# Kernel tuning notes

Measured on AMD Instinct MI355X. Metric: run time of the kernel, lower is better.

## Reference

```python
import jax, jax.numpy as jnp
import numpy as np

# ---- Config constants (from DGM Config) ----
DIM = 20        # number of assets; inputs have DIM+1 cols (last is time)
DELTA = 0.01    # finite-difference step / covariance scale
RHO = 0.5       # asset correlation
MC = 32         # Config.mc_num
N = 2048        # interior points (inputs holds 2*N rows)
UNITS = 128     # Config.unit_num
LAYERS = 3      # Config.layer_num
SIG = 0.2       # Config._sig
MU = 0.05       # Config._mu
R = 0.05        # Config._r

_cov = DELTA * (np.full((DIM, DIM), RHO, dtype=np.float64) + (1.0 - RHO) * np.eye(DIM))
L_TRIL = jnp.asarray(np.linalg.cholesky(_cov).astype(np.float32))  # (DIM, DIM) lower-tri


def setup_inputs() -> dict:
    key = jax.random.key(0)
    ks = jax.random.split(key, 20)
    d = DIM + 1
    u = lambda k, shp: jax.random.uniform(k, shp, jnp.float32, -0.05, 0.05)
    inp = {
        # strictly positive inputs so boundary prod**(1/DIM) is well-defined
        "inputs": jax.random.uniform(ks[0], (2 * N, d), jnp.float32, 0.1, 1.0),
        "eps": jax.random.normal(ks[1], (MC, N, DIM), jnp.float32),
        "w1": u(ks[2], (d, UNITS)), "b1": u(ks[3], (UNITS,)),
        "uzl": u(ks[4], (d, UNITS)), "wzl": u(ks[5], (UNITS, UNITS)), "bzl": u(ks[6], (UNITS,)),
        "ugl": u(ks[7], (d, UNITS)), "wgl": u(ks[8], (UNITS, UNITS)), "bgl": u(ks[9], (UNITS,)),
        "url": u(ks[10], (d, UNITS)), "wrl": u(ks[11], (UNITS, UNITS)), "brl": u(ks[12], (UNITS,)),
        "uhl": u(ks[13], (d, UNITS)), "whl": u(ks[14], (UNITS, UNITS)), "bhl": u(ks[15], (UNITS,)),
        "w": u(ks[16], (UNITS, 1)), "b": u(ks[17], (1,)),
    }
    return inp


def _value(x, w1, b1, uzl, wzl, bzl, ugl, wgl, bgl, url, wrl, brl, uhl, whl, bhl, w, b):
    # DGM gated residual network; x: (..., DIM+1) -> (..., 1)
    act = jnp.tanh
    s = act(x @ w1 + b1)
    for _ in range(LAYERS):
        z = act(x @ uzl + s @ wzl + bzl)
        g = act(x @ ugl + s @ wgl + bgl)
        r = act(x @ url + s @ wrl + brl)
        h = act(x @ uhl + (s * r) @ whl + bhl)
        s = (1.0 - g) * h + z * s
    return s @ w + b


def reference(inputs, eps, w1, b1, uzl, wzl, bzl, ugl, wgl, bgl, url, wrl, brl,
              uhl, whl, bhl, w, b):
    params = (w1, b1, uzl, wzl, bzl, ugl, wgl, bgl, url, wrl, brl, uhl, whl, bhl, w, b)
    val = lambda x: _value(x, *params)
    x1, x2 = jnp.split(inputs, 2, axis=0)          # interior / boundary points

    # first-order grad of value w.r.t. interior inputs
    fprime = jax.grad(lambda x: val(x).sum())(x1)  # (N, DIM+1)
    drift = jnp.concatenate([MU * x1[:, :-1], jnp.ones((x1.shape[0], 1), x1.dtype)], axis=1)
    term1_1 = jnp.sum(drift * fprime, axis=1)      # (N,)

    # correlated MVN perturbations (reparameterized): loc + eps @ L^T
    loc = x1[:, :-1]                               # (N, DIM)
    sample = loc[None, :, :] + jnp.einsum('mnd,kd->mnk', eps, L_TRIL)  # (MC, N, DIM)
    xdiff = sample * (SIG * loc)[None, :, :]
    violation = jnp.concatenate([xdiff, jnp.zeros((MC, x1.shape[0], 1), x1.dtype)], axis=2)
    xplus = x1[None, :, :] + violation             # (MC, N, DIM+1)

    fprime_plus = jax.grad(lambda x: val(x).sum())(xplus)  # (MC, N, DIM+1)
    term1_2 = jnp.sum(
        jnp.mean((fprime_plus - fprime[None, :, :]) / DELTA * violation, axis=0), axis=1)

    # boundary residual: value - payoff (geometric-mean call payoff)
    payoff = jax.nn.relu(jnp.power(jnp.prod(x2[:, :-1], axis=1), 1.0 / DIM))
    term2 = jnp.squeeze(val(x2), -1) - payoff

    interior = term1_1 + 0.5 * term1_2 - R * jnp.squeeze(val(x1), -1)
    return jnp.concatenate([interior, term2], axis=0)  # (2N,)
```

## Files before the change

### kernel.cpp

```cpp
#include <hip/hip_runtime.h>
#include <math.h>

#define DIMN 20
#define DD 21
#define NN 2048
#define MCN 32
#define UNITS 128
#define SIGC 0.2f
#define MUC 0.05f
#define RC 0.05f
#define DELTAC 0.01f

#define TM 32
#define KCH 16
#define KC3 8
#define PTOT (NN + MCN*NN + NN)
#define NBLK (PTOT/TM)

#define OFF_L 0
#define OFF_WT 512
#define OFF_UZGR (OFF_WT + 4*16384)
#define OFF_WZGR (OFF_UZGR + 8192)
#define OFF_FP1  (OFF_WZGR + 49152)
#define OFF_VAL1 (OFF_FP1 + NN*DD)
#define OFF_VAL2 (OFF_VAL1 + NN)
#define OFF_T12  (OFF_VAL2 + NN)
#define OFF_GATES (OFF_T12 + NN)

#define ST_S1 0
#define ST_Z1 4096
#define ST_G1 8192
#define ST_R1 12288
#define ST_Z2 16384
#define ST_G2 20480
#define ST_R2 24576
#define GB_STRIDE 28672

#define L_TOT_SG 19776
#define L_TOT_RC 23872

#define ELT44(...) _Pragma("unroll") for (int p = 0; p < 4; p++){ _Pragma("unroll") for (int jj = 0; jj < 4; jj++){ __VA_ARGS__; } }

__device__ __forceinline__ int offq(int row, int p0){
    return row*32 + ((p0 + 4*(row&7)) & 31);
}
__device__ __forceinline__ int offs(int row, int p){
    return row*32 + (((p & 28) + 4*(row&7)) & 31) + (p & 3);
}

__device__ __forceinline__ void stageW(const float* __restrict__ g, float* wc, int units){
#if defined(__has_builtin) && __has_builtin(__builtin_amdgcn_global_load_lds)
    int lane = threadIdx.x & 63, wid = threadIdx.x >> 6;
    for (int base = wid*64; base < units; base += 256){
        int u = base + lane;
        if (u < units)
            __builtin_amdgcn_global_load_lds(
                (const __attribute__((address_space(1))) unsigned int*)(g) + (size_t)u*4,
                (__attribute__((address_space(3))) unsigned int*)(wc) + (size_t)base*4,
                16, 0, 0);
    }
#else
    int t = threadIdx.x;
    for (int u = t; u < units; u += 256){
        float4 v = *(const float4*)(g + u*4);
        *(float4*)(wc + u*4) = v;
    }
#endif
}

#define FMA16(acc, s4, w4) \
  acc[0][0]=fmaf(s4.x,w4.x,acc[0][0]); acc[0][1]=fmaf(s4.x,w4.y,acc[0][1]); \
  acc[0][2]=fmaf(s4.x,w4.z,acc[0][2]); acc[0][3]=fmaf(s4.x,w4.w,acc[0][3]); \
  acc[1][0]=fmaf(s4.y,w4.x,acc[1][0]); acc[1][1]=fmaf(s4.y,w4.y,acc[1][1]); \
  acc[1][2]=fmaf(s4.y,w4.z,acc[1][2]); acc[1][3]=fmaf(s4.y,w4.w,acc[1][3]); \
  acc[2][0]=fmaf(s4.z,w4.x,acc[2][0]); acc[2][1]=fmaf(s4.z,w4.y,acc[2][1]); \
  acc[2][2]=fmaf(s4.z,w4.z,acc[2][2]); acc[2][3]=fmaf(s4.z,w4.w,acc[2][3]); \
  acc[3][0]=fmaf(s4.w,w4.x,acc[3][0]); acc[3][1]=fmaf(s4.w,w4.y,acc[3][1]); \
  acc[3][2]=fmaf(s4.w,w4.z,acc[3][2]); acc[3][3]=fmaf(s4.w,w4.w,acc[3][3]);

__device__ __forceinline__ void mm_acc(const float* __restrict__ gW, int K,
    const float* __restrict__ vec, float acc[4][4], float* __restrict__ Wc,
    int jg, int p0)
{
    int nch = (K + KCH - 1) / KCH;
    {
        int r0 = (K < KCH) ? K : KCH;
        stageW(gW, Wc, r0*32);
    }
    for (int c = 0; c < nch; c++){
        __syncthreads();
        if (c + 1 < nch){
            int c0n = (c+1)*KCH;
            int rn = K - c0n; if (rn > KCH) rn = KCH;
            stageW(gW + c0n*UNITS, Wc + ((c+1)&1)*KCH*UNITS, rn*32);
        }
        int c0 = c*KCH;
        int rows = K - c0; if (rows > KCH) rows = KCH;
        const float* wb = Wc + (c&1)*KCH*UNITS;
        if (rows == KCH){
            #pragma unroll 4
            for (int kk = 0; kk < KCH; kk++){
                int k = c0 + kk;
                float4 w4 = *(const float4*)(wb + kk*UNITS + 4*jg);
                float4 s4 = *(const float4*)(vec + offq(k, p0));
                FMA16(acc, s4, w4)
            }
        } else {
            for (int kk = 0; kk < rows; kk++){
                int k = c0 + kk;
                float4 w4 = *(const float4*)(wb + kk*UNITS + 4*jg);
                float4 s4 = *(const float4*)(vec + offq(k, p0));
                FMA16(acc, s4, w4)
            }
        }
    }
    __syncthreads();
}

__device__ __forceinline__ void mm3_acc(const float* __restrict__ gW, int K,
    const float* __restrict__ vec, float az[4][4], float ag[4][4], float ar[4][4],
    float* __restrict__ Wc, int jg, int p0)
{
    int nch = (K + KC3 - 1) / KC3;
    {
        int r0 = (K < KC3) ? K : KC3;
        stageW(gW, Wc, r0*96);
    }
    for (int c = 0; c < nch; c++){
        __syncthreads();
        if (c + 1 < nch){
            int c0n = (c+1)*KC3;
            int rn = K - c0n; if (rn > KC3) rn = KC3;
            stageW(gW + c0n*384, Wc + ((c+1)&1)*(KC3*384), rn*96);
        }
        int c0 = c*KC3;
        int rows = K - c0; if (rows > KC3) rows = KC3;
        const float* wb = Wc + (c&1)*(KC3*384);
        if (rows == KC3){
            #pragma unroll 2
            for (int kk = 0; kk < KC3; kk++){
                int k = c0 + kk;
                const float* wrow = wb + kk*384 + 4*jg;
                float4 s4  = *(const float4*)(vec + offq(k, p0));
                float4 wz4 = *(const float4*)(wrow);
                float4 wg4 = *(const float4*)(wrow + 128);
                float4 wr4 = *(const float4*)(wrow + 256);
                FMA16(az, s4, wz4)
                FMA16(ag, s4, wg4)
                FMA16(ar, s4, wr4)
            }
        } else {
            for (int kk = 0; kk < rows; kk++){
                int k = c0 + kk;
                const float* wrow = wb + kk*384 + 4*jg;
                float4 s4  = *(const float4*)(vec + offq(k, p0));
                float4 wz4 = *(const float4*)(wrow);
                float4 wg4 = *(const float4*)(wrow + 128);
                float4 wr4 = *(const float4*)(wrow + 256);
                FMA16(az, s4, wz4)
                FMA16(ag, s4, wg4)
                FMA16(ar, s4, wr4)
            }
        }
    }
    __syncthreads();
}

__device__ __forceinline__ void write_own(float* buf, const float v[4][4], int j0, int p0){
    #pragma unroll
    for (int jj = 0; jj < 4; jj++){
        int j = j0 + jj;
        float4 q = make_float4(v[0][jj], v[1][jj], v[2][jj], v[3][jj]);
        *(float4*)(buf + offq(j, p0)) = q;
    }
}
__device__ __forceinline__ void read_own(const float* buf, float v[4][4], int j0, int p0){
    #pragma unroll
    for (int jj = 0; jj < 4; jj++){
        int j = j0 + jj;
        float4 q = *(const float4*)(buf + offq(j, p0));
        v[0][jj]=q.x; v[1][jj]=q.y; v[2][jj]=q.z; v[3][jj]=q.w;
    }
}
__device__ __forceinline__ void stash_w(float* buf, const float v[4][4], int t){
    #pragma unroll
    for (int jj = 0; jj < 4; jj++)
        *(float4*)(buf + (jj*256 + t)*4) = make_float4(v[0][jj], v[1][jj], v[2][jj], v[3][jj]);
}
__device__ __forceinline__ void stash_r(const float* buf, float v[4][4], int t){
    #pragma unroll
    for (int jj = 0; jj < 4; jj++){
        float4 q = *(const float4*)(buf + (jj*256 + t)*4);
        v[0][jj]=q.x; v[1][jj]=q.y; v[2][jj]=q.z; v[3][jj]=q.w;
    }
}

__device__ __forceinline__ void gate_f(const float* __restrict__ U, const float* __restrict__ W,
    const float* __restrict__ bias, const float* __restrict__ xT, const float* __restrict__ Sin,
    float* __restrict__ Wc, float out[4][4], int jg, int p0, int j0)
{
    float acc[4][4];
    float4 b = *(const float4*)(bias + j0);
    #pragma unroll
    for (int p = 0; p < 4; p++){ acc[p][0]=b.x; acc[p][1]=b.y; acc[p][2]=b.z; acc[p][3]=b.w; }
    mm_acc(U, DD, xT, acc, Wc, jg, p0);
    mm_acc(W, UNITS, Sin, acc, Wc, jg, p0);
    #pragma unroll
    for (int p = 0; p < 4; p++)
        #pragma unroll
        for (int jj = 0; jj < 4; jj++) out[p][jj] = tanhf(acc[p][jj]);
}

__device__ __forceinline__ void gate3_f(const float* __restrict__ Uzgr, const float* __restrict__ Wzgr,
    const float* __restrict__ bz, const float* __restrict__ bg, const float* __restrict__ br,
    const float* __restrict__ xT, const float* __restrict__ Sin,
    float* __restrict__ Wc, float zt[4][4], float gt[4][4], float rt[4][4],
    int jg, int p0, int j0)
{
    float4 b0 = *(const float4*)(bz + j0);
    float4 b1 = *(const float4*)(bg + j0);
    float4 b2 = *(const float4*)(br + j0);
    #pragma unroll
    for (int p = 0; p < 4; p++){
        zt[p][0]=b0.x; zt[p][1]=b0.y; zt[p][2]=b0.z; zt[p][3]=b0.w;
        gt[p][0]=b1.x; gt[p][1]=b1.y; gt[p][2]=b1.z; gt[p][3]=b1.w;
        rt[p][0]=b2.x; rt[p][1]=b2.y; rt[p][2]=b2.z; rt[p][3]=b2.w;
    }
    mm3_acc(Uzgr, DD, xT, zt, gt, rt, Wc, jg, p0);
    mm3_acc(Wzgr, UNITS, Sin, zt, gt, rt, Wc, jg, p0);
    ELT44(zt[p][jj]=tanhf(zt[p][jj]); gt[p][jj]=tanhf(gt[p][jj]); rt[p][jj]=tanhf(rt[p][jj]))
}

__global__ void chol_kernel(float* __restrict__ Lout)
{
    if (threadIdx.x == 0 && blockIdx.x == 0) {
        const double beta = 0.01 * 0.5;
        const double diag = 0.01;
        double c[DIMN], d[DIMN];
        double S = 0.0;
        for (int j = 0; j < DIMN; j++){
            double dj = sqrt(diag - S);
            double cj = (beta - S) / dj;
            d[j] = dj; c[j] = cj;
            S += cj*cj;
        }
        for (int i = 0; i < DIMN; i++)
            for (int j = 0; j < DIMN; j++)
                Lout[i*DIMN + j] = (j < i) ? (float)c[j] : (j == i) ? (float)d[i] : 0.0f;
    }
}

__global__ void transpose_k(const float* __restrict__ wz, const float* __restrict__ wg,
                            const float* __restrict__ wr, const float* __restrict__ wh,
                            float* __restrict__ WT)
{
    int idx = blockIdx.x*256 + threadIdx.x;
    int q = idx >> 14, r2 = idx & 16383, k = r2 >> 7, j = r2 & 127;
    const float* src = (q==0)? wz : (q==1)? wg : (q==2)? wr : wh;
    WT[(q<<14) + j*UNITS + k] = src[k*UNITS + j];
}

__global__ void pack_zgr(const float* __restrict__ uz, const float* __restrict__ ug,
                         const float* __restrict__ ur,
                         const float* __restrict__ wz, const float* __restrict__ wg,
                         const float* __restrict__ wr,
                         float* __restrict__ Uzgr, float* __restrict__ Wzgr)
{
    int idx = blockIdx.x*256 + threadIdx.x;
    if (idx < 128*384){
        int k = idx/384, c = idx - k*384, g = c >> 7, j = c & 127;
        const float* s = (g==0)? wz : (g==1)? wg : wr;
        Wzgr[idx] = s[k*UNITS + j];
        return;
    }
    int i2 = idx - 128*384;
    if (i2 < 21*384){
        int k = i2/384, c = i2 - k*384, g = c >> 7, j = c & 127;
        const float* s = (g==0)? uz : (g==1)? ug : ur;
        Uzgr[i2] = s[k*UNITS + j];
    }
}

#define DGM_PARAMS \
    const float* __restrict__ inputs, const float* __restrict__ eps, \
    const float* __restrict__ w1, const float* __restrict__ b1, \
    const float* __restrict__ uz, const float* __restrict__ bz, \
    const float* __restrict__ ug, const float* __restrict__ bg, \
    const float* __restrict__ ur, const float* __restrict__ br, \
    const float* __restrict__ uh, const float* __restrict__ wh, const float* __restrict__ bh, \
    const float* __restrict__ wv, const float* __restrict__ bv, \
    const float* __restrict__ Lm, const float* __restrict__ WT, \
    const float* __restrict__ Uzgr, const float* __restrict__ Wzgr, \
    float* __restrict__ gws, \
    float* __restrict__ fp1, float* __restrict__ val1, float* __restrict__ val2, \
    float* __restrict__ t12acc

#define DGM_ARGS inputs, eps, w1, b1, uz, bz, ug, bg, ur, br, uh, wh, bh, wv, bv, \
    Lm, WT, Uzgr, Wzgr, gws, fp1, val1, val2, t12acc

template<int SG>
__device__ __forceinline__ void dgm_body(float* lds, DGM_PARAMS)
{
    float* S0 = lds;
    float* S1 = SG ? lds : lds + 4096;
    float* S2 = lds + (SG ? 4096 : 8192);
    float* Db = lds + (SG ? 8192 : 12288);
    float* Wc = lds + (SG ? 12288 : 16384);
    float* xT = lds + (SG ? 18432 : 22528);
    float* Vb = lds + (SG ? 19104 : 23200);

    const int t  = threadIdx.x;
    const int jg = t & 31;
    const int pg = t >> 5;
    const int p0 = pg * 4;
    const int j0 = jg * 4;
    const int P0 = blockIdx.x * TM;
    const int type = (P0 < NN) ? 0 : (P0 < NN + MCN*NN) ? 1 : 2;
    int base_n = 0, mrow = 0;
    if (type == 1){ int q = P0 - NN; mrow = q >> 11; base_n = q & (NN-1); }

    float* gb = gws + (size_t)blockIdx.x * GB_STRIDE;

    {
        int p = t & 31, kq = t >> 5;
        for (int ki = 0; ki < 3; ki++){
            int k = kq + 8*ki;
            if (k > DIMN) break;
            float xv;
            if (type == 0){
                xv = inputs[(P0 + p)*DD + k];
            } else if (type == 2){
                xv = inputs[(NN + (P0 - NN - MCN*NN) + p)*DD + k];
            } else {
                int n = base_n + p;
                float x1v = inputs[n*DD + k];
                if (k == DIMN) xv = x1v;
                else {
                    const float* ep = eps + (size_t)(mrow*NN + n)*DIMN;
                    float a = x1v;
                    for (int d = 0; d < DIMN; d++) a = fmaf(ep[d], Lm[k*DIMN + d], a);
                    float viol = a * (SIGC * x1v);
                    Vb[offs(k, p)] = viol;
                    xv = x1v + viol;
                }
            }
            xT[offs(k, p)] = xv;
        }
    }
    __syncthreads();

    float s_own[4][4];
    {
        float acc[4][4];
        float4 b = *(const float4*)(b1 + j0);
        #pragma unroll
        for (int p = 0; p < 4; p++){ acc[p][0]=b.x; acc[p][1]=b.y; acc[p][2]=b.z; acc[p][3]=b.w; }
        mm_acc(w1, DD, xT, acc, Wc, jg, p0);
        ELT44(s_own[p][jj] = tanhf(acc[p][jj]))
        write_own(S0, s_own, j0, p0);
        __syncthreads();
    }

    float zt[4][4], gt[4][4], rt[4][4], ht[4][4];

#define GATES(SIN, SMUL) \
    gate3_f(Uzgr, Wzgr, bz, bg, br, xT, SIN, Wc, zt, gt, rt, jg, p0, j0); \
    { float tt[4][4]; ELT44(tt[p][jj] = SMUL[p][jj]*rt[p][jj]) write_own(Db, tt, j0, p0); } \
    gate_f(uh, wh, bh, xT, Db, Wc, ht, jg, p0, j0);

#define FWD_LAYER(SIN) \
    GATES(SIN, s_own) \
    ELT44(s_own[p][jj] = (1.f - gt[p][jj])*ht[p][jj] + zt[p][jj]*s_own[p][jj])

    FWD_LAYER(S0)
    if (SG){ if (type != 2){
        stash_w(gb + ST_S1, s_own, t);
        stash_w(gb + ST_Z1, zt, t); stash_w(gb + ST_G1, gt, t); stash_w(gb + ST_R1, rt, t);
    } }
    else   { write_own(S1, s_own, j0, p0); }
    write_own(Db, s_own, j0, p0);

    FWD_LAYER(Db)
    if (SG && type != 2){
        stash_w(gb + ST_Z2, zt, t); stash_w(gb + ST_G2, gt, t); stash_w(gb + ST_R2, rt, t);
    }
    write_own(S2, s_own, j0, p0);

    FWD_LAYER(S2)

    {
        float4 wv4 = *(const float4*)(wv + j0);
        float vs[4];
        #pragma unroll
        for (int p = 0; p < 4; p++)
            vs[p] = s_own[p][0]*wv4.x + s_own[p][1]*wv4.y + s_own[p][2]*wv4.z + s_own[p][3]*wv4.w;
        __syncthreads();
        *(float4*)(Db + jg*32 + p0) = make_float4(vs[0], vs[1], vs[2], vs[3]);
        __syncthreads();
        if (t < TM){
            float v = bv[0];
            for (int j2 = 0; j2 < 32; j2++) v += Db[j2*32 + t];
            if (type == 0) val1[P0 + t] = v;
            else if (type == 2) val2[P0 + t - NN - MCN*NN] = v;
        }
        __syncthreads();
    }
    if (type == 2) return;

    float ds[4][4];
    {
        float4 wv4 = *(const float4*)(wv + j0);
        #pragma unroll
        for (int p = 0; p < 4; p++){ ds[p][0]=wv4.x; ds[p][1]=wv4.y; ds[p][2]=wv4.z; ds[p][3]=wv4.w; }
    }
    float proj[4] = {0.f, 0.f, 0.f, 0.f};
    float dxp[3] = {0.f, 0.f, 0.f};
    const int pi = t >> 3, il = t & 7;

    const float* WTz = WT;
    const float* WTg = WT + 16384;
    const float* WTr = WT + 2*16384;
    const float* WTh = WT + 3*16384;

#define DX_DOT(UMAT) \
    { _Pragma("unroll") for (int ii = 0; ii < 3; ii++){ \
        int i = il + 8*ii; \
        if (i < DD){ \
            const float* Urow = UMAT + i*UNITS; \
            float a = 0.f; \
            for (int j2 = 0; j2 < UNITS; j2++) a = fmaf(Db[offs(j2, pi)], Urow[j2], a); \
            dxp[ii] += a; \
        } } }

#define PROJ_D(UMAT, SEL) \
    { float uv[4][4]; \
      ELT44(uv[p][jj] = 0.f) \
      const float* up_ = UMAT + 4*jg; \
      _Pragma("unroll 4") \
      for (int k = 0; k < DIMN; k++){ \
          float4 w4 = *(const float4*)(up_ + k*UNITS); \
          float4 s4 = *(const float4*)(Vb + offq(k, p0)); \
          FMA16(uv, s4, w4) \
      } \
      ELT44(proj[p] += uv[p][jj]*SEL[p][jj]) }

#define BWD_LAYER(SLP, MODE, GZ, GG, GR) \
    { \
    float dsn[4][4]; \
    if (MODE == 1){ \
        float slg[4][4]; read_own(SLP, slg, j0, p0); \
        GATES(SLP, slg) \
    } \
    {  \
        float sl[4][4], zv[4][4]; \
        if (MODE == 2){ stash_r(gb + ST_S1, sl, t); stash_r(gb + GZ, zv, t); } \
        else if (MODE == 3){ read_own(SLP, sl, j0, p0); stash_r(gb + GZ, zv, t); } \
        else if (MODE == 0){ read_own(S2, sl, j0, p0); ELT44(zv[p][jj] = zt[p][jj]) } \
        else { read_own(SLP, sl, j0, p0); ELT44(zv[p][jj] = zt[p][jj]) } \
        float dzp[4][4]; \
        ELT44(float d=ds[p][jj]; float zz=zv[p][jj]; \
            dzp[p][jj] = d*sl[p][jj]*(1.f - zz*zz); dsn[p][jj] = d*zz) \
        write_own(Db, dzp, j0, p0); \
        if (type == 1){ PROJ_D(uz, dzp) } else { __syncthreads(); DX_DOT(uz) } \
    } \
    mm_acc(WTz, UNITS, Db, dsn, Wc, jg, p0); \
    float dhp[4][4]; \
    {  \
        float gv[4][4], hv[4][4]; \
        if (MODE == 2 || MODE == 3){ \
            float zv[4][4], sl[4][4], sn[4][4]; \
            stash_r(gb + GZ, zv, t); stash_r(gb + GG, gv, t); \
            if (MODE == 2){ stash_r(gb + ST_S1, sl, t); read_own(S2, sn, j0, p0); } \
            else { read_own(SLP, sl, j0, p0); stash_r(gb + ST_S1, sn, t); } \
            ELT44(hv[p][jj] = (sn[p][jj] - zv[p][jj]*sl[p][jj]) / (1.f - gv[p][jj])) \
        } else { ELT44(gv[p][jj] = gt[p][jj]; hv[p][jj] = ht[p][jj]) } \
        float dgp[4][4]; \
        ELT44(float d=ds[p][jj]; float gg=gv[p][jj]; float hh=hv[p][jj]; \
            dgp[p][jj] = -d*hh*(1.f - gg*gg); \
            dhp[p][jj] = d*(1.f - gg)*(1.f - hh*hh)) \
        write_own(Db, dgp, j0, p0); \
        if (type == 1){ PROJ_D(ug, dgp) } else { __syncthreads(); DX_DOT(ug) } \
    } \
    mm_acc(WTg, UNITS, Db, dsn, Wc, jg, p0); \
    write_own(Db, dhp, j0, p0); \
    if (type == 1){ PROJ_D(uh, dhp) } else { __syncthreads(); DX_DOT(uh) } \
    float dsr[4][4]; \
    ELT44(dsr[p][jj] = 0.f) \
    mm_acc(WTh, UNITS, Db, dsr, Wc, jg, p0); \
    {  \
        float rv[4][4], sl[4][4], drp[4][4]; \
        if (MODE == 2){ stash_r(gb + GR, rv, t); stash_r(gb + ST_S1, sl, t); } \
        else if (MODE == 3){ stash_r(gb + GR, rv, t); read_own(SLP, sl, j0, p0); } \
        else if (MODE == 0){ ELT44(rv[p][jj] = rt[p][jj]) read_own(S2, sl, j0, p0); } \
        else { ELT44(rv[p][jj] = rt[p][jj]) read_own(SLP, sl, j0, p0); } \
        ELT44(float dr=dsr[p][jj]; float rr=rv[p][jj]; \
            drp[p][jj] = dr*sl[p][jj]*(1.f - rr*rr); dsn[p][jj] += dr*rr) \
        write_own(Db, drp, j0, p0); \
        if (type == 1){ PROJ_D(ur, drp) } else { __syncthreads(); DX_DOT(ur) } \
    } \
    mm_acc(WTr, UNITS, Db, dsn, Wc, jg, p0); \
    ELT44(ds[p][jj] = dsn[p][jj]) \
    }

    BWD_LAYER(S0, 0, ST_Z2, ST_G2, ST_R2)
    BWD_LAYER(S1, (SG ? 2 : 1), ST_Z2, ST_G2, ST_R2)
    if (SG){ BWD_LAYER(S0, 3, ST_Z1, ST_G1, ST_R1) }
    else   { BWD_LAYER(S0, 1, ST_Z1, ST_G1, ST_R1) }

    {
        float s0l[4][4];
        read_own(S0, s0l, j0, p0);
        float v0[4][4];
        ELT44(v0[p][jj] = ds[p][jj]*(1.f - s0l[p][jj]*s0l[p][jj]))

        if (type == 1){
            PROJ_D(w1, v0)
            __syncthreads();
            *(float4*)(Db + jg*32 + p0) = make_float4(proj[0], proj[1], proj[2], proj[3]);
            __syncthreads();
            if (t < TM){
                float s = 0.f;
                for (int j2 = 0; j2 < 32; j2++) s += Db[j2*32 + t];
                atomicAdd(t12acc + base_n + t, s);
            }
        } else {
            write_own(Db, v0, j0, p0);
            __syncthreads();
            DX_DOT(w1)
            #pragma unroll
            for (int ii = 0; ii < 3; ii++){
                int i = il + 8*ii;
                if (i < DD) fp1[(P0 + pi)*DD + i] = dxp[ii];
            }
        }
    }
}

__global__ __launch_bounds__(256) __attribute__((amdgpu_waves_per_eu(2,2))) void dgm_sg(DGM_PARAMS){
    __shared__ float lds[L_TOT_SG];
    dgm_body<1>(lds, DGM_ARGS);
}
__global__ __launch_bounds__(256) __attribute__((amdgpu_waves_per_eu(2,2))) void dgm_rc(DGM_PARAMS){
    __shared__ float lds[L_TOT_RC];
    dgm_body<0>(lds, DGM_ARGS);
}

__global__ void finalize_k(const float* __restrict__ inputs, const float* __restrict__ eps,
    const float* __restrict__ Lm, const float* __restrict__ fp1, const float* __restrict__ val1,
    const float* __restrict__ val2, const float* __restrict__ t12acc, float* __restrict__ out)
{
    int n = blockIdx.x*256 + threadIdx.x;
    if (n >= NN) return;
    float fp[DD];
    #pragma unroll
    for (int k = 0; k < DD; k++) fp[k] = fp1[n*DD + k];
    float t11 = fp[DIMN];
    #pragma unroll
    for (int k = 0; k < DIMN; k++) t11 = fmaf(MUC*inputs[n*DD + k], fp[k], t11);
    float esum[DIMN];
    #pragma unroll
    for (int d = 0; d < DIMN; d++){
        float a = 0.f;
        for (int m = 0; m < MCN; m++) a += eps[(size_t)(m*NN + n)*DIMN + d];
        esum[d] = a;
    }
    float t12b = 0.f;
    #pragma unroll
    for (int k = 0; k < DIMN; k++){
        float loc = inputs[n*DD + k];
        float ssum = (float)MCN * loc;
        #pragma unroll
        for (int d = 0; d < DIMN; d++) ssum = fmaf(esum[d], Lm[k*DIMN + d], ssum);
        float vsum = ssum * (SIGC*loc);
        t12b = fmaf(fp[k], vsum, t12b);
    }
    float term12 = (t12acc[n] - t12b) * (1.0f/(DELTAC*(float)MCN));
    out[n] = t11 + 0.5f*term12 - RC*val1[n];

    float prod = 1.f;
    #pragma unroll
    for (int k = 0; k < DIMN; k++) prod *= inputs[(NN + n)*DD + k];
    float payoff = powf(prod, 1.0f/(float)DIMN);
    if (!(payoff > 0.f)) payoff = 0.f;
    out[NN + n] = val2[n] - payoff;
}

extern "C" void kernel_launch(void* const* d_in, const int* in_sizes, int n_in,
                              void* d_out, int out_size, void* d_ws, size_t ws_size,
                              hipStream_t stream)
{
    const float* inputs = (const float*)d_in[0];
    const float* eps    = (const float*)d_in[1];
    const float* w1     = (const float*)d_in[2];
    const float* b1     = (const float*)d_in[3];
    const float* uz     = (const float*)d_in[4];
    const float* wz     = (const float*)d_in[5];
    const float* bz     = (const float*)d_in[6];
    const float* ug     = (const float*)d_in[7];
    const float* wg     = (const float*)d_in[8];
    const float* bg     = (const float*)d_in[9];
    const float* urr    = (const float*)d_in[10];
    const float* wr     = (const float*)d_in[11];
    const float* br     = (const float*)d_in[12];
    const float* uh     = (const float*)d_in[13];
    const float* wh     = (const float*)d_in[14];
    const float* bh     = (const float*)d_in[15];
    const float* wv     = (const float*)d_in[16];
    const float* bv     = (const float*)d_in[17];

    float* ws    = (float*)d_ws;
    float* Lm    = ws + OFF_L;
    float* WT    = ws + OFF_WT;
    float* Uzgr  = ws + OFF_UZGR;
    float* Wzgr  = ws + OFF_WZGR;
    float* fp1   = ws + OFF_FP1;
    float* val1  = ws + OFF_VAL1;
    float* val2  = ws + OFF_VAL2;
    float* t12   = ws + OFF_T12;
    float* gates = ws + OFF_GATES;
    float* out   = (float*)d_out;

    hipMemsetAsync(t12, 0, NN*sizeof(float), stream);
    hipLaunchKernelGGL(chol_kernel, dim3(1), dim3(64), 0, stream, Lm);
    hipLaunchKernelGGL(transpose_k, dim3(256), dim3(256), 0, stream, wz, wg, wr, wh, WT);
    hipLaunchKernelGGL(pack_zgr, dim3(224), dim3(256), 0, stream, uz, ug, urr, wz, wg, wr, Uzgr, Wzgr);

    size_t need_bytes = ((size_t)OFF_GATES + (size_t)NBLK * (size_t)GB_STRIDE) * sizeof(float);
    if (ws_size >= need_bytes){
        hipLaunchKernelGGL(dgm_sg, dim3(NBLK), dim3(256), 0, stream,
            inputs, eps, w1, b1, uz, bz, ug, bg, urr, br, uh, wh, bh, wv, bv,
            Lm, WT, Uzgr, Wzgr, gates, fp1, val1, val2, t12);
    } else {
        hipLaunchKernelGGL(dgm_rc, dim3(NBLK), dim3(256), 0, stream,
            inputs, eps, w1, b1, uz, bz, ug, bg, urr, br, uh, wh, bh, wv, bv,
            Lm, WT, Uzgr, Wzgr, gates, fp1, val1, val2, t12);
    }
    hipLaunchKernelGGL(finalize_k, dim3(8), dim3(256), 0, stream,
        inputs, eps, Lm, fp1, val1, val2, t12, out);
}
```

Before: 1.371 ms.

## Read small input-weight matrices directly from global, use fast tanh, enlarge K chunk

```diff
diff --git a/kernel.cpp b/kernel.cpp
--- a/kernel.cpp
+++ b/kernel.cpp
@@ -12,7 +12,7 @@
 #define DELTAC 0.01f
 
 #define TM 32
-#define KCH 16
+#define KCH 24
 #define KC3 8
 #define PTOT (NN + MCN*NN + NN)
 #define NBLK (PTOT/TM)
@@ -46,6 +46,12 @@
 }
 __device__ __forceinline__ int offs(int row, int p){
     return row*32 + (((p & 28) + 4*(row&7)) & 31) + (p & 3);
+}
+
+__device__ __forceinline__ float ftanh(float x){
+    float cx = fminf(9.f, fmaxf(-9.f, x));
+    float e  = __expf(2.f*cx);
+    return fmaf(-2.f, __builtin_amdgcn_rcpf(e + 1.f), 1.f);
 }
 
 __device__ __forceinline__ void stageW(const float* __restrict__ g, float* wc, int units){
@@ -77,6 +83,33 @@
   acc[2][2]=fmaf(s4.z,w4.z,acc[2][2]); acc[2][3]=fmaf(s4.z,w4.w,acc[2][3]); \
   acc[3][0]=fmaf(s4.w,w4.x,acc[3][0]); acc[3][1]=fmaf(s4.w,w4.y,acc[3][1]); \
   acc[3][2]=fmaf(s4.w,w4.z,acc[3][2]); acc[3][3]=fmaf(s4.w,w4.w,acc[3][3]);
+
+__device__ __forceinline__ void mmU_d(const float* __restrict__ gU, int K,
+    const float* __restrict__ vec, float acc[4][4], int jg, int p0)
+{
+    const float* up = gU + 4*jg;
+    #pragma unroll 4
+    for (int k = 0; k < K; k++){
+        float4 w4 = *(const float4*)(up + k*UNITS);
+        float4 s4 = *(const float4*)(vec + offq(k, p0));
+        FMA16(acc, s4, w4)
+    }
+}
+__device__ __forceinline__ void mmU3_d(const float* __restrict__ gU, int K,
+    const float* __restrict__ vec, float a0[4][4], float a1[4][4], float a2[4][4],
+    int jg, int p0)
+{
+    const float* up = gU + 4*jg;
+    #pragma unroll 2
+    for (int k = 0; k < K; k++){
+        const float* r = up + k*384;
+        float4 s4 = *(const float4*)(vec + offq(k, p0));
+        float4 w0 = *(const float4*)(r);
+        float4 w1v = *(const float4*)(r + 128);
+        float4 w2 = *(const float4*)(r + 256);
+        FMA16(a0, s4, w0) FMA16(a1, s4, w1v) FMA16(a2, s4, w2)
+    }
+}
 
 __device__ __forceinline__ void mm_acc(const float* __restrict__ gW, int K,
     const float* __restrict__ vec, float acc[4][4], float* __restrict__ Wc,
@@ -203,12 +236,12 @@
     float4 b = *(const float4*)(bias + j0);
     #pragma unroll
     for (int p = 0; p < 4; p++){ acc[p][0]=b.x; acc[p][1]=b.y; acc[p][2]=b.z; acc[p][3]=b.w; }
-    mm_acc(U, DD, xT, acc, Wc, jg, p0);
+    mmU_d(U, DD, xT, acc, jg, p0);
     mm_acc(W, UNITS, Sin, acc, Wc, jg, p0);
     #pragma unroll
     for (int p = 0; p < 4; p++)
         #pragma unroll
-        for (int jj = 0; jj < 4; jj++) out[p][jj] = tanhf(acc[p][jj]);
+        for (int jj = 0; jj < 4; jj++) out[p][jj] = ftanh(acc[p][jj]);
 }
 
 __device__ __forceinline__ void gate3_f(const float* __restrict__ Uzgr, const float* __restrict__ Wzgr,
@@ -226,9 +259,9 @@
         gt[p][0]=b1.x; gt[p][1]=b1.y; gt[p][2]=b1.z; gt[p][3]=b1.w;
         rt[p][0]=b2.x; rt[p][1]=b2.y; rt[p][2]=b2.z; rt[p][3]=b2.w;
     }
-    mm3_acc(Uzgr, DD, xT, zt, gt, rt, Wc, jg, p0);
+    mmU3_d(Uzgr, DD, xT, zt, gt, rt, jg, p0);
     mm3_acc(Wzgr, UNITS, Sin, zt, gt, rt, Wc, jg, p0);
-    ELT44(zt[p][jj]=tanhf(zt[p][jj]); gt[p][jj]=tanhf(gt[p][jj]); rt[p][jj]=tanhf(rt[p][jj]))
+    ELT44(zt[p][jj]=ftanh(zt[p][jj]); gt[p][jj]=ftanh(gt[p][jj]); rt[p][jj]=ftanh(rt[p][jj]))
 }
 
 __global__ void chol_kernel(float* __restrict__ Lout)
@@ -355,8 +388,8 @@
         float4 b = *(const float4*)(b1 + j0);
         #pragma unroll
         for (int p = 0; p < 4; p++){ acc[p][0]=b.x; acc[p][1]=b.y; acc[p][2]=b.z; acc[p][3]=b.w; }
-        mm_acc(w1, DD, xT, acc, Wc, jg, p0);
-        ELT44(s_own[p][jj] = tanhf(acc[p][jj]))
+        mmU_d(w1, DD, xT, acc, jg, p0);
+        ELT44(s_own[p][jj] = ftanh(acc[p][jj]))
         write_own(S0, s_own, j0, p0);
         __syncthreads();
     }
@@ -435,13 +468,7 @@
 #define PROJ_D(UMAT, SEL) \
     { float uv[4][4]; \
       ELT44(uv[p][jj] = 0.f) \
-      const float* up_ = UMAT + 4*jg; \
-      _Pragma("unroll 4") \
-      for (int k = 0; k < DIMN; k++){ \
-          float4 w4 = *(const float4*)(up_ + k*UNITS); \
-          float4 s4 = *(const float4*)(Vb + offq(k, p0)); \
-          FMA16(uv, s4, w4) \
-      } \
+      mmU_d(UMAT, DIMN, Vb, uv, jg, p0); \
       ELT44(proj[p] += uv[p][jj]*SEL[p][jj]) }
 
 #define BWD_LAYER(SLP, MODE, GZ, GG, GR) \
```

After: 1.306 ms. 4.8% less time.
